# Kernel tuning notes

Hardware: AMD Instinct MI355X
Metric: run time of the kernel (lower is better)

The kernel has to match this reference:

```python
import math
import jax, jax.numpy as jnp
import numpy as np

EMBED_DIM = 1024
NUM_HEADS = 16
HEAD_DIM = EMBED_DIM // NUM_HEADS
NUM_BUCKETS = 32
MAX_DISTANCE = 128


def _relative_position_bucket(relative_position, num_buckets=NUM_BUCKETS, max_distance=MAX_DISTANCE):
    # Bidirectional T5 bucketing (matches torch reference exactly).
    num_buckets = num_buckets // 2
    relative_buckets = (relative_position > 0).astype(jnp.int32) * num_buckets
    relative_position = jnp.abs(relative_position)
    max_exact = num_buckets // 2
    is_small = relative_position < max_exact
    rp_large = jnp.log(relative_position.astype(jnp.float32) / max_exact) / math.log(max_distance / max_exact)
    rp_large = max_exact + (rp_large * (num_buckets - max_exact)).astype(jnp.int32)
    rp_large = jnp.minimum(rp_large, num_buckets - 1)
    relative_buckets = relative_buckets + jnp.where(is_small, relative_position, rp_large)
    return relative_buckets


def compute_bias(rel_emb, query_length, key_length):
    context_position = jnp.arange(query_length, dtype=jnp.int32)[:, None]
    memory_position = jnp.arange(key_length, dtype=jnp.int32)[None, :]
    relative_position = memory_position - context_position  # [q, k]
    buckets = _relative_position_bucket(relative_position)
    values = rel_emb[buckets]                 # [q, k, h]
    return jnp.transpose(values, (2, 0, 1))[None]  # [1, h, q, k]


def setup_inputs() -> dict:
    key = jax.random.key(0)
    k1, k2, k3, k4 = jax.random.split(key, 4)
    B, S = 2, 2048
    hidden_states = jax.random.normal(k1, (B, S, EMBED_DIM), dtype=jnp.float32)
    scale = 1.0 / math.sqrt(EMBED_DIM)
    W_qkv = jax.random.normal(k2, (EMBED_DIM, 3 * EMBED_DIM), dtype=jnp.float32) * scale
    W_out = jax.random.normal(k3, (EMBED_DIM, EMBED_DIM), dtype=jnp.float32) * scale
    rel_emb = jax.random.normal(k4, (NUM_BUCKETS, NUM_HEADS), dtype=jnp.float32) * 0.02
    return {"hidden_states": hidden_states, "W_qkv": W_qkv, "W_out": W_out, "rel_emb": rel_emb}


def reference(hidden_states, W_qkv, W_out, rel_emb):
    B, S, _ = hidden_states.shape
    qkv = hidden_states @ W_qkv                                # [B, S, 3*D]
    qkv = qkv.reshape(B, S, 3, NUM_HEADS, HEAD_DIM)
    qkv = jnp.transpose(qkv, (0, 3, 2, 1, 4))                  # [B, H, 3, S, dh]
    q, k, v = qkv[:, :, 0], qkv[:, :, 1], qkv[:, :, 2]
    scores = jnp.einsum('bhqd,bhkd->bhqk', q, k)               # no 1/sqrt(d) scaling (T5 style)
    scores = scores + compute_bias(rel_emb, S, S)
    attn = jax.nn.softmax(scores.astype(jnp.float32), axis=-1).astype(scores.dtype)
    out = jnp.einsum('bhqk,bhkd->bhqd', attn, v)               # [B, H, S, dh]
    out = jnp.transpose(out, (0, 2, 1, 3)).reshape(B, S, EMBED_DIM)
    return out @ W_out
```

## Files before the change

### kernel.cpp

```cpp
#include <hip/hip_runtime.h>
#include <hip/hip_bf16.h>
#include <math.h>

typedef _Float16 f16;
typedef __attribute__((ext_vector_type(8))) _Float16 f16x8;
typedef __attribute__((ext_vector_type(4))) _Float16 f16x4;
typedef __attribute__((ext_vector_type(4))) float f32x4;

#define EMBED 1024
#define NHEADS 16
#define HDIM 64
#define BATCH 2
#define SEQ 2048
#define BS 4096
#define LOG2E 1.4426950408889634f


__device__ __forceinline__ f32x4 mfma16x32(f16x8 a, f16x8 b, f32x4 c) {
  return __builtin_amdgcn_mfma_f32_16x16x32_f16(a, b, c, 0, 0, 0);
}
__device__ __forceinline__ f32x4 mfma16x16(f16x4 a, f16x4 b, f32x4 c) {
  return __builtin_amdgcn_mfma_f32_16x16x16f16(a, b, c, 0, 0, 0);
}
__device__ __forceinline__ void gload_lds16(const f16* __restrict__ g, f16* l) {
  __builtin_amdgcn_global_load_lds(
      (const __attribute__((address_space(1))) void*)g,
      (__attribute__((address_space(3))) void*)l, 16, 0, 0);
}

__global__ void cast_x_kernel(const float* __restrict__ src, f16* __restrict__ dst) {
  int i = (blockIdx.x * 256 + threadIdx.x) * 4;
  float4 v = *(const float4*)(src + i);
  f16x4 o = { (f16)v.x, (f16)v.y, (f16)v.z, (f16)v.w };
  *(f16x4*)(dst + i) = o;
}

__global__ void transpose_cast_kernel(const float* __restrict__ in, f16* __restrict__ out,
                                      int K, int N) {
  __shared__ float tile[32][33];
  int n0 = blockIdx.x * 32, k0 = blockIdx.y * 32;
  int tx = threadIdx.x & 31, ty = threadIdx.x >> 5;
#pragma unroll
  for (int r = ty; r < 32; r += 8) tile[r][tx] = in[(size_t)(k0 + r) * N + n0 + tx];
  __syncthreads();
#pragma unroll
  for (int r = ty; r < 32; r += 8) out[(size_t)(n0 + r) * K + k0 + tx] = (f16)tile[tx][r];
}

__global__ void bias_table_kernel(const float* __restrict__ rel_emb, float* __restrict__ btab) {
  int idx = blockIdx.x * 256 + threadIdx.x;
  if (idx >= 4095) return;
  int rp = idx - 2047;
  int rb = rp > 0 ? 16 : 0;
  int arp = rp < 0 ? -rp : rp;
  int loc;
  if (arp < 8) {
    loc = arp;
  } else {
    float lr = logf((float)arp * 0.125f) * (1.0f / 2.7725887222397811f);
    int t = 8 + (int)(lr * 8.0f);
    loc = t < 15 ? t : 15;
  }
  int bucket = rb + loc;
#pragma unroll
  for (int h = 0; h < 16; h++) btab[h * 4095 + idx] = rel_emb[bucket * 16 + h] * LOG2E;
}

__device__ __forceinline__ void gemm_core(const f16* __restrict__ A, const f16* __restrict__ Bt,
                                          int m0, int n0, int Kdim, f32x4 (&acc)[4][4]) {
  __shared__ __align__(16) f16 As[128 * 32];
  __shared__ __align__(16) f16 Bs[128 * 32];

  int tid = threadIdx.x;
  int lane = tid & 63, wave = tid >> 6;
  int l15 = lane & 15, quad = lane >> 4;
  int wr = (wave >> 1) * 64, wc = (wave & 1) * 64;
  int rowl = lane >> 2;
  int col8 = (lane & 3) * 8;

#pragma unroll
  for (int i = 0; i < 4; i++)
#pragma unroll
    for (int j = 0; j < 4; j++) acc[i][j] = f32x4{0.f, 0.f, 0.f, 0.f};

  for (int kt = 0; kt < Kdim / 32; kt++) {
    int kk = kt * 32;
#pragma unroll
    for (int c = 0; c < 2; c++) {
      int row = wave * 32 + c * 16 + rowl;
      gload_lds16(A + (size_t)(m0 + row) * Kdim + kk + col8, &As[(wave * 32 + c * 16) * 32]);
      gload_lds16(Bt + (size_t)(n0 + row) * Kdim + kk + col8, &Bs[(wave * 32 + c * 16) * 32]);
    }
    __syncthreads();
    f16x8 af[4], bf[4];
#pragma unroll
    for (int i = 0; i < 4; i++) af[i] = *(const f16x8*)(&As[(wr + i * 16 + l15) * 32 + quad * 8]);
#pragma unroll
    for (int j = 0; j < 4; j++) bf[j] = *(const f16x8*)(&Bs[(wc + j * 16 + l15) * 32 + quad * 8]);
#pragma unroll
    for (int i = 0; i < 4; i++)
#pragma unroll
      for (int j = 0; j < 4; j++) acc[i][j] = mfma16x32(af[i], bf[j], acc[i][j]);
    __syncthreads();
  }
}

__global__ __launch_bounds__(256, 2) void gemm_qkv_kernel(
    const f16* __restrict__ Xh, const f16* __restrict__ Wt,
    f16* __restrict__ Q, f16* __restrict__ K_, f16* __restrict__ Vp) {
  f32x4 acc[4][4];
  int m0 = blockIdx.y * 128, n0 = blockIdx.x * 128;
  gemm_core(Xh, Wt, m0, n0, 1024, acc);

  int lane = threadIdx.x & 63, wave = threadIdx.x >> 6;
  int l15 = lane & 15, quad = lane >> 4;
  int wr = (wave >> 1) * 64, wc = (wave & 1) * 64;
  int nq = n0 + wc;
  int which = nq >> 10;
  int h = (nq >> 6) & 15;
  int b = m0 >> 11;

  if (which == 2) {
    int s0 = (m0 & 2047) + wr;
    f16* vbase = Vp + (size_t)(b * 16 + h) * 131072 + (size_t)(s0 >> 6) * 4096;
#pragma unroll
    for (int i = 0; i < 4; i++) {
#pragma unroll
      for (int jp = 0; jp < 2; jp++) {
        f16x8 pk = { (f16)acc[i][2 * jp][0],     (f16)acc[i][2 * jp][1],
                     (f16)acc[i][2 * jp][2],     (f16)acc[i][2 * jp][3],
                     (f16)acc[i][2 * jp + 1][0], (f16)acc[i][2 * jp + 1][1],
                     (f16)acc[i][2 * jp + 1][2], (f16)acc[i][2 * jp + 1][3] };
        *(f16x8*)(vbase + (i * 2 + jp) * 512 + lane * 8) = pk;
      }
    }
  } else {
    f16* base = (which == 0) ? Q : K_;
    float sc = (which == 0) ? LOG2E : 1.0f;
#pragma unroll
    for (int i = 0; i < 4; i++) {
#pragma unroll
      for (int j = 0; j < 4; j++) {
        int d = j * 16 + l15;
#pragma unroll
        for (int r = 0; r < 4; r++) {
          int m = m0 + wr + i * 16 + quad * 4 + r;
          int s = m & 2047;
          base[(((size_t)(b * 16 + h) * 2048 + s) << 6) + d] = (f16)(acc[i][j][r] * sc);
        }
      }
    }
  }
}

__global__ void repack_k_kernel(const f16* __restrict__ Kw, f16* __restrict__ Kp) {
  int o = blockIdx.x * 256 + threadIdx.x;
  int lane = o & 63;
  int ct = (o >> 6) & 7;
  int kt = (o >> 9) & 31;
  int bh = o >> 14;
  int c = ct >> 1, t = ct & 1;
  int l15 = lane & 15, quad = lane >> 4;
  int s = kt * 64 + c * 16 + l15;
  f16x8 v = *(const f16x8*)(Kw + ((size_t)(bh * 2048 + s) << 6) + t * 32 + quad * 8);
  *(f16x8*)(Kp + (size_t)o * 8) = v;
}

__global__ __launch_bounds__(256, 4) void attn_kernel(
    const f16* __restrict__ Q, const f16* __restrict__ Kp, const f16* __restrict__ Vp,
    const float* __restrict__ btab, f16* __restrict__ O) {
  __shared__ __align__(16) float bias4[4][2116];

  int qt = blockIdx.x, bh = blockIdx.y;
  int qbase = qt * 64;
  int h = bh & 15, b = bh >> 4;
  int tid = threadIdx.x, lane = tid & 63, wave = tid >> 6;
  int l15 = lane & 15, quad = lane >> 4;

  const float* brow = btab + h * 4095 + (1984 - qbase);
#pragma unroll
  for (int j = 0; j < 4; j++)
    for (int i = tid; i < 2116; i += 256) {
      int src = i + j;
      bias4[j][i] = (src <= 2110) ? brow[src] : 0.f;
    }

  const f16* qptr = Q + ((size_t)bh * 2048 + qbase + wave * 16 + l15) * 64 + quad * 8;
  f16x8 qf0 = *(const f16x8*)(qptr);
  f16x8 qf1 = *(const f16x8*)(qptr + 32);

  f32x4 accO[4] = {};
  float m_i = -INFINITY, l_i = 0.f;

  const f16* kpp = Kp + (size_t)bh * 131072;
  const f16* vpp = Vp + (size_t)bh * 131072;
  const int bofs = quad * 4 - wave * 16 - l15 + 63;

  __syncthreads();

  for (int kt = 0; kt < 32; kt++) {
    const f16* kptr = kpp + kt * 4096;
    const f16* vptr = vpp + kt * 4096;
    int kb = kt * 64;
    f32x4 scT[4];
#pragma unroll
    for (int c = 0; c < 4; c++) {
      int bi = kb + c * 16 + bofs;
      int bj = bi & 3;
      scT[c] = *(const f32x4*)(&bias4[bj][bi - bj]);
      f16x8 kf0 = *(const f16x8*)(kptr + (c * 2 + 0) * 512 + lane * 8);
      f16x8 kf1 = *(const f16x8*)(kptr + (c * 2 + 1) * 512 + lane * 8);
      scT[c] = mfma16x32(kf0, qf0, scT[c]);
      scT[c] = mfma16x32(kf1, qf1, scT[c]);
    }
    f16x8 vf8[4][2];
#pragma unroll
    for (int c = 0; c < 4; c++)
#pragma unroll
      for (int jp = 0; jp < 2; jp++)
        vf8[c][jp] = *(const f16x8*)(vptr + (c * 2 + jp) * 512 + lane * 8);
    float mc[4];
#pragma unroll
    for (int c = 0; c < 4; c++)
      mc[c] = fmaxf(fmaxf(scT[c][0], scT[c][1]), fmaxf(scT[c][2], scT[c][3]));
    float mx = fmaxf(fmaxf(fmaxf(mc[0], mc[1]), fmaxf(mc[2], mc[3])), m_i);
    mx = fmaxf(mx, __shfl_xor(mx, 16));
    mx = fmaxf(mx, __shfl_xor(mx, 32));
    float alpha = exp2f(m_i - mx);
    m_i = mx;
    f16x4 p[4];
    float rc[4];
#pragma unroll
    for (int c = 0; c < 4; c++) {
      float e0 = exp2f(scT[c][0] - mx);
      float e1 = exp2f(scT[c][1] - mx);
      float e2 = exp2f(scT[c][2] - mx);
      float e3 = exp2f(scT[c][3] - mx);
      rc[c] = (e0 + e1) + (e2 + e3);
      p[c][0] = (f16)e0; p[c][1] = (f16)e1; p[c][2] = (f16)e2; p[c][3] = (f16)e3;
    }
    float rs = (rc[0] + rc[1]) + (rc[2] + rc[3]);
    rs += __shfl_xor(rs, 16);
    rs += __shfl_xor(rs, 32);
    l_i = l_i * alpha + rs;
    float arow[4];
#pragma unroll
    for (int r = 0; r < 4; r++) arow[r] = __shfl(alpha, quad * 4 + r);
#pragma unroll
    for (int d = 0; d < 4; d++)
#pragma unroll
      for (int r = 0; r < 4; r++) accO[d][r] *= arow[r];
#pragma unroll
    for (int c = 0; c < 4; c++) {
#pragma unroll
      for (int jp = 0; jp < 2; jp++) {
        f16x4 vlo = __builtin_shufflevector(vf8[c][jp], vf8[c][jp], 0, 1, 2, 3);
        f16x4 vhi = __builtin_shufflevector(vf8[c][jp], vf8[c][jp], 4, 5, 6, 7);
        accO[2 * jp]     = mfma16x16(p[c], vlo, accO[2 * jp]);
        accO[2 * jp + 1] = mfma16x16(p[c], vhi, accO[2 * jp + 1]);
      }
    }
  }

  float linv = 1.0f / l_i;
  float lrow[4];
#pragma unroll
  for (int r = 0; r < 4; r++) lrow[r] = __shfl(linv, quad * 4 + r);
#pragma unroll
  for (int dblk = 0; dblk < 4; dblk++) {
#pragma unroll
    for (int r = 0; r < 4; r++) {
      int q = qbase + wave * 16 + quad * 4 + r;
      O[((size_t)(b * 2048 + q) << 10) + h * 64 + dblk * 16 + l15] = (f16)(accO[dblk][r] * lrow[r]);
    }
  }
}

__global__ __launch_bounds__(256, 2) void gemm_out_kernel(
    const f16* __restrict__ Oh, const f16* __restrict__ Wt, float* __restrict__ out) {
  f32x4 acc[4][4];
  int m0 = blockIdx.y * 128, n0 = blockIdx.x * 128;
  gemm_core(Oh, Wt, m0, n0, 1024, acc);

  int lane = threadIdx.x & 63, wave = threadIdx.x >> 6;
  int l15 = lane & 15, quad = lane >> 4;
  int wr = (wave >> 1) * 64, wc = (wave & 1) * 64;
#pragma unroll
  for (int i = 0; i < 4; i++) {
#pragma unroll
    for (int j = 0; j < 4; j++) {
      int n = n0 + wc + j * 16 + l15;
#pragma unroll
      for (int r = 0; r < 4; r++) {
        int m = m0 + wr + i * 16 + quad * 4 + r;
        out[((size_t)m << 10) + n] = acc[i][j][r];
      }
    }
  }
}

extern "C" void kernel_launch(void* const* d_in, const int* in_sizes, int n_in,
                              void* d_out, int out_size, void* d_ws, size_t ws_size,
                              hipStream_t stream) {
  const float* X = (const float*)d_in[0];
  const float* Wqkv = (const float*)d_in[1];
  const float* Wout = (const float*)d_in[2];
  const float* rel = (const float*)d_in[3];

  char* ws = (char*)d_ws;
  f16* Xh     = (f16*)(ws + 0);
  f16* Kp     = (f16*)(ws + 0);
  f16* Wqkv_t = (f16*)(ws + 8388608);
  f16* Wout_t = (f16*)(ws + 14680064);
  f16* Qw     = (f16*)(ws + 16777216);
  f16* Kw     = (f16*)(ws + 25165824);
  f16* Vp     = (f16*)(ws + 33554432);
  f16* Ow     = (f16*)(ws + 41943040);
  float* btab = (float*)(ws + 50331648);

  cast_x_kernel<<<4096, 256, 0, stream>>>(X, Xh);
  transpose_cast_kernel<<<dim3(96, 32), 256, 0, stream>>>(Wqkv, Wqkv_t, 1024, 3072);
  transpose_cast_kernel<<<dim3(32, 32), 256, 0, stream>>>(Wout, Wout_t, 1024, 1024);
  bias_table_kernel<<<16, 256, 0, stream>>>(rel, btab);
  gemm_qkv_kernel<<<dim3(24, 32), 256, 0, stream>>>(Xh, Wqkv_t, Qw, Kw, Vp);
  repack_k_kernel<<<2048, 256, 0, stream>>>(Kw, Kp);
  attn_kernel<<<dim3(32, 32), 256, 0, stream>>>(Qw, Kp, Vp, btab, Ow);
  gemm_out_kernel<<<dim3(8, 32), 256, 0, stream>>>(Ow, Wout_t, (float*)d_out);
}
```

Before: 234.3 us.

## Merge prep kernels into one launch and add lazy softmax rescaling in attention

Merges the X cast, both weight transpose-casts and the bias-table build into one prep kernel, removing three launches. In attention, the four shifted bias copies in LDS become one unshifted array read with scalar loads. The running max and the rescaling of the accumulator and row sum now happen only when some lane sees a new maximum (a wave-uniform branch), and K/V pointers are advanced incrementally. The trade-off is unaligned scalar LDS bias reads in place of vector reads, plus branch overhead.

```diff
diff --git a/kernel.cpp b/kernel.cpp
--- a/kernel.cpp
+++ b/kernel.cpp
@@ -28,42 +28,49 @@
       (__attribute__((address_space(3))) void*)l, 16, 0, 0);
 }
 
-__global__ void cast_x_kernel(const float* __restrict__ src, f16* __restrict__ dst) {
-  int i = (blockIdx.x * 256 + threadIdx.x) * 4;
-  float4 v = *(const float4*)(src + i);
-  f16x4 o = { (f16)v.x, (f16)v.y, (f16)v.z, (f16)v.w };
-  *(f16x4*)(dst + i) = o;
-}
-
-__global__ void transpose_cast_kernel(const float* __restrict__ in, f16* __restrict__ out,
-                                      int K, int N) {
+__global__ void prep_kernel(const float* __restrict__ X, const float* __restrict__ Wqkv,
+                            const float* __restrict__ Wout, const float* __restrict__ rel_emb,
+                            f16* __restrict__ Xh, f16* __restrict__ Wqkv_t,
+                            f16* __restrict__ Wout_t, float* __restrict__ btab) {
   __shared__ float tile[32][33];
-  int n0 = blockIdx.x * 32, k0 = blockIdx.y * 32;
-  int tx = threadIdx.x & 31, ty = threadIdx.x >> 5;
-#pragma unroll
-  for (int r = ty; r < 32; r += 8) tile[r][tx] = in[(size_t)(k0 + r) * N + n0 + tx];
-  __syncthreads();
-#pragma unroll
-  for (int r = ty; r < 32; r += 8) out[(size_t)(n0 + r) * K + k0 + tx] = (f16)tile[tx][r];
-}
-
-__global__ void bias_table_kernel(const float* __restrict__ rel_emb, float* __restrict__ btab) {
-  int idx = blockIdx.x * 256 + threadIdx.x;
-  if (idx >= 4095) return;
-  int rp = idx - 2047;
-  int rb = rp > 0 ? 16 : 0;
-  int arp = rp < 0 ? -rp : rp;
-  int loc;
-  if (arp < 8) {
-    loc = arp;
+  int bid = blockIdx.x, tid = threadIdx.x;
+  if (bid < 4096) {
+    int i = (bid * 256 + tid) * 4;
+    float4 v = *(const float4*)(X + i);
+    f16x4 o = { (f16)v.x, (f16)v.y, (f16)v.z, (f16)v.w };
+    *(f16x4*)(Xh + i) = o;
+  } else if (bid < 8192) {
+    const float* in;
+    f16* out;
+    int N, idx;
+    if (bid < 7168) { in = Wqkv; out = Wqkv_t; N = 3072; idx = bid - 4096; }
+    else            { in = Wout; out = Wout_t; N = 1024; idx = bid - 7168; }
+    int nt = N / 32;
+    int n0 = (idx % nt) * 32, k0 = (idx / nt) * 32;
+    int tx = tid & 31, ty = tid >> 5;
+#pragma unroll
+    for (int r = ty; r < 32; r += 8) tile[r][tx] = in[(size_t)(k0 + r) * N + n0 + tx];
+    __syncthreads();
+#pragma unroll
+    for (int r = ty; r < 32; r += 8) out[(size_t)(n0 + r) * 1024 + k0 + tx] = (f16)tile[tx][r];
   } else {
-    float lr = logf((float)arp * 0.125f) * (1.0f / 2.7725887222397811f);
-    int t = 8 + (int)(lr * 8.0f);
-    loc = t < 15 ? t : 15;
-  }
-  int bucket = rb + loc;
-#pragma unroll
-  for (int h = 0; h < 16; h++) btab[h * 4095 + idx] = rel_emb[bucket * 16 + h] * LOG2E;
+    int idx = (bid - 8192) * 256 + tid;
+    if (idx >= 4095) return;
+    int rp = idx - 2047;
+    int rb = rp > 0 ? 16 : 0;
+    int arp = rp < 0 ? -rp : rp;
+    int loc;
+    if (arp < 8) {
+      loc = arp;
+    } else {
+      float lr = logf((float)arp * 0.125f) * (1.0f / 2.7725887222397811f);
+      int t = 8 + (int)(lr * 8.0f);
+      loc = t < 15 ? t : 15;
+    }
+    int bucket = rb + loc;
+#pragma unroll
+    for (int h = 0; h < 16; h++) btab[h * 4095 + idx] = rel_emb[bucket * 16 + h] * LOG2E;
+  }
 }
 
 __device__ __forceinline__ void gemm_core(const f16* __restrict__ A, const f16* __restrict__ Bt,
@@ -169,7 +176,7 @@
 __global__ __launch_bounds__(256, 4) void attn_kernel(
     const f16* __restrict__ Q, const f16* __restrict__ Kp, const f16* __restrict__ Vp,
     const float* __restrict__ btab, f16* __restrict__ O) {
-  __shared__ __align__(16) float bias4[4][2116];
+  __shared__ float bias_lds[2112];
 
   int qt = blockIdx.x, bh = blockIdx.y;
   int qbase = qt * 64;
@@ -178,12 +185,7 @@
   int l15 = lane & 15, quad = lane >> 4;
 
   const float* brow = btab + h * 4095 + (1984 - qbase);
-#pragma unroll
-  for (int j = 0; j < 4; j++)
-    for (int i = tid; i < 2116; i += 256) {
-      int src = i + j;
-      bias4[j][i] = (src <= 2110) ? brow[src] : 0.f;
-    }
+  for (int i = tid; i < 2111; i += 256) bias_lds[i] = brow[i];
 
   const f16* qptr = Q + ((size_t)bh * 2048 + qbase + wave * 16 + l15) * 64 + quad * 8;
   f16x8 qf0 = *(const f16x8*)(qptr);
@@ -192,24 +194,21 @@
   f32x4 accO[4] = {};
   float m_i = -INFINITY, l_i = 0.f;
 
-  const f16* kpp = Kp + (size_t)bh * 131072;
-  const f16* vpp = Vp + (size_t)bh * 131072;
+  const f16* kc = Kp + (size_t)bh * 131072 + 1792;
+  const f16* vc = Vp + (size_t)bh * 131072 + 1792;
+  const int voff = lane * 8;
   const int bofs = quad * 4 - wave * 16 - l15 + 63;
 
   __syncthreads();
 
   for (int kt = 0; kt < 32; kt++) {
-    const f16* kptr = kpp + kt * 4096;
-    const f16* vptr = vpp + kt * 4096;
-    int kb = kt * 64;
+    const float* bb = &bias_lds[kt * 64 + bofs];
     f32x4 scT[4];
 #pragma unroll
     for (int c = 0; c < 4; c++) {
-      int bi = kb + c * 16 + bofs;
-      int bj = bi & 3;
-      scT[c] = *(const f32x4*)(&bias4[bj][bi - bj]);
-      f16x8 kf0 = *(const f16x8*)(kptr + (c * 2 + 0) * 512 + lane * 8);
-      f16x8 kf1 = *(const f16x8*)(kptr + (c * 2 + 1) * 512 + lane * 8);
+      scT[c] = f32x4{ bb[c * 16], bb[c * 16 + 1], bb[c * 16 + 2], bb[c * 16 + 3] };
+      f16x8 kf0 = *(const f16x8*)(kc + ((c * 2 + 0) * 512 - 1792) + voff);
+      f16x8 kf1 = *(const f16x8*)(kc + ((c * 2 + 1) * 512 - 1792) + voff);
       scT[c] = mfma16x32(kf0, qf0, scT[c]);
       scT[c] = mfma16x32(kf1, qf1, scT[c]);
     }
@@ -218,16 +217,28 @@
     for (int c = 0; c < 4; c++)
 #pragma unroll
       for (int jp = 0; jp < 2; jp++)
-        vf8[c][jp] = *(const f16x8*)(vptr + (c * 2 + jp) * 512 + lane * 8);
-    float mc[4];
-#pragma unroll
-    for (int c = 0; c < 4; c++)
-      mc[c] = fmaxf(fmaxf(scT[c][0], scT[c][1]), fmaxf(scT[c][2], scT[c][3]));
-    float mx = fmaxf(fmaxf(fmaxf(mc[0], mc[1]), fmaxf(mc[2], mc[3])), m_i);
-    mx = fmaxf(mx, __shfl_xor(mx, 16));
-    mx = fmaxf(mx, __shfl_xor(mx, 32));
-    float alpha = exp2f(m_i - mx);
-    m_i = mx;
+        vf8[c][jp] = *(const f16x8*)(vc + ((c * 2 + jp) * 512 - 1792) + voff);
+    float mp0 = fmaxf(fmaxf(scT[0][0], scT[0][1]), fmaxf(scT[0][2], scT[0][3]));
+    float mp1 = fmaxf(fmaxf(scT[1][0], scT[1][1]), fmaxf(scT[1][2], scT[1][3]));
+    float mp2 = fmaxf(fmaxf(scT[2][0], scT[2][1]), fmaxf(scT[2][2], scT[2][3]));
+    float mp3 = fmaxf(fmaxf(scT[3][0], scT[3][1]), fmaxf(scT[3][2], scT[3][3]));
+    float mp = fmaxf(fmaxf(mp0, mp1), fmaxf(mp2, mp3));
+    if (__any(mp > m_i)) {
+      float mx = fmaxf(mp, __shfl_xor(mp, 16));
+      mx = fmaxf(mx, __shfl_xor(mx, 32));
+      float mn = fmaxf(m_i, mx);
+      float alpha = exp2f(m_i - mn);
+      m_i = mn;
+      l_i *= alpha;
+      float arow[4];
+#pragma unroll
+      for (int r = 0; r < 4; r++) arow[r] = __shfl(alpha, quad * 4 + r);
+#pragma unroll
+      for (int d = 0; d < 4; d++)
+#pragma unroll
+        for (int r = 0; r < 4; r++) accO[d][r] *= arow[r];
+    }
+    float mx = m_i;
     f16x4 p[4];
     float rc[4];
 #pragma unroll
@@ -242,14 +253,7 @@
     float rs = (rc[0] + rc[1]) + (rc[2] + rc[3]);
     rs += __shfl_xor(rs, 16);
     rs += __shfl_xor(rs, 32);
-    l_i = l_i * alpha + rs;
-    float arow[4];
-#pragma unroll
-    for (int r = 0; r < 4; r++) arow[r] = __shfl(alpha, quad * 4 + r);
-#pragma unroll
-    for (int d = 0; d < 4; d++)
-#pragma unroll
-      for (int r = 0; r < 4; r++) accO[d][r] *= arow[r];
+    l_i += rs;
 #pragma unroll
     for (int c = 0; c < 4; c++) {
 #pragma unroll
@@ -260,6 +264,8 @@
         accO[2 * jp + 1] = mfma16x16(p[c], vhi, accO[2 * jp + 1]);
       }
     }
+    kc += 4096;
+    vc += 4096;
   }
 
   float linv = 1.0f / l_i;
@@ -318,10 +324,7 @@
   f16* Ow     = (f16*)(ws + 41943040);
   float* btab = (float*)(ws + 50331648);
 
-  cast_x_kernel<<<4096, 256, 0, stream>>>(X, Xh);
-  transpose_cast_kernel<<<dim3(96, 32), 256, 0, stream>>>(Wqkv, Wqkv_t, 1024, 3072);
-  transpose_cast_kernel<<<dim3(32, 32), 256, 0, stream>>>(Wout, Wout_t, 1024, 1024);
-  bias_table_kernel<<<16, 256, 0, stream>>>(rel, btab);
+  prep_kernel<<<8208, 256, 0, stream>>>(X, Wqkv, Wout, rel, Xh, Wqkv_t, Wout_t, btab);
   gemm_qkv_kernel<<<dim3(24, 32), 256, 0, stream>>>(Xh, Wqkv_t, Qw, Kw, Vp);
   repack_k_kernel<<<2048, 256, 0, stream>>>(Kw, Kp);
   attn_kernel<<<dim3(32, 32), 256, 0, stream>>>(Qw, Kp, Vp, btab, Ow);
```

New measurement: 223.6 us. 1.05x faster.
